# Kernel tuning notes

Hardware: AMD Instinct MI355X
Metric: run time of the kernel (lower is better)

The kernel has to match this reference:

```python
import jax, jax.numpy as jnp
import numpy as np

B, N, D, F, L, R = 16, 1024, 256, 128, 2, 2


def setup_inputs() -> dict:
    key = jax.random.key(0)
    ks = jax.random.split(key, 12)
    s = 0.05
    return {
        "node_embed": jax.random.normal(ks[0], (B, N, D), jnp.float32),
        "input_x": jax.random.normal(ks[1], (B, F), jnp.float32),
        "adj": jax.random.randint(ks[2], (R, B, N, N), 0, 2, jnp.int32),
        "WQi_w": jax.random.normal(ks[3], (L, F, F), jnp.float32) * s,
        "WQi_b": jnp.zeros((L, F), jnp.float32),
        "WQ_w": jax.random.normal(ks[4], (L, D + F, D), jnp.float32) * s,
        "WQ_b": jnp.zeros((L, D), jnp.float32),
        "WK_w": jax.random.normal(ks[5], (L, R, D + F, D), jnp.float32) * s,
        "WK_b": jnp.zeros((L, R, D), jnp.float32),
        "WV_w": jax.random.normal(ks[6], (L, R, D + F, D), jnp.float32) * s,
        "WV_b": jnp.zeros((L, R, D), jnp.float32),
        "WF_w": jax.random.normal(ks[7], (L, R * D, D), jnp.float32) * s,
        "WF_b": jnp.zeros((L, D), jnp.float32),
        "ln_g": jnp.ones((L, D), jnp.float32),
        "ln_b": jnp.zeros((L, D), jnp.float32),
    }


def _layer_norm(x, g, b, eps=1e-5):
    mu = jnp.mean(x, axis=-1, keepdims=True)
    var = jnp.var(x, axis=-1, keepdims=True)
    return (x - mu) * jax.lax.rsqrt(var + eps) * g + b


def reference(node_embed, input_x, adj, WQi_w, WQi_b, WQ_w, WQ_b,
              WK_w, WK_b, WV_w, WV_b, WF_w, WF_b, ln_g, ln_b):
    scale = 1.0 / (D ** 0.5)
    h = node_embed
    for l in range(L):
        # input feature projection, broadcast over nodes
        x1 = input_x @ WQi_w[l] + WQi_b[l]              # (B, F)
        x1 = jnp.broadcast_to(x1[:, None, :], (h.shape[0], h.shape[1], F))
        qc = jnp.concatenate([h, x1], axis=-1)          # (B, N, D+F)
        q = qc @ WQ_w[l] + WQ_b[l]                      # (B, N, D)
        outs = []
        for r in range(R):
            k = qc @ WK_w[l, r] + WK_b[l, r]            # (B, N, D)
            v = qc @ WV_w[l, r] + WV_b[l, r]            # (B, N, D)
            scores = jnp.einsum('bnd,bmd->bnm', q, k) * scale
            scores = jnp.where(adj[r] == 0, -1e9, scores)
            alpha = jax.nn.softmax(scores, axis=-1)
            outs.append(jnp.einsum('bnm,bmd->bnd', alpha, v))
        h_concat = jnp.concatenate(outs, axis=-1)       # (B, N, R*D)
        h_fused = jax.nn.relu(h_concat @ WF_w[l] + WF_b[l])
        h = _layer_norm(h + h_fused, ln_g[l], ln_b[l])
    return h
```

## Files before the change

kernel.cpp:

```cpp
#include <hip/hip_runtime.h>
#include <hip/hip_bf16.h>

#define BB 16
#define NN 1024
#define DD 256
#define FF_ 128
#define LL 2
#define RR 2
#define DF 384
#define MM (BB*NN)
#define NPROJ 1280
#define PK 768

typedef __attribute__((ext_vector_type(8))) short s16x8;
typedef __attribute__((ext_vector_type(4))) float f32x4;
typedef __attribute__((ext_vector_type(16))) float f32x16;
typedef __attribute__((ext_vector_type(2))) unsigned int u32x2;
typedef __attribute__((ext_vector_type(4))) unsigned int u32x4;
typedef __attribute__((ext_vector_type(4))) unsigned short us16x4;

__device__ __forceinline__ unsigned short f2bf(float f){
  unsigned u = __builtin_bit_cast(unsigned, f);
  u += 0x7fff + ((u >> 16) & 1);
  return (unsigned short)(u >> 16);
}

__device__ __forceinline__ void gload16(const void* g, void* l){
  __builtin_amdgcn_global_load_lds(
      (const __attribute__((address_space(1))) unsigned int*)g,
      (__attribute__((address_space(3))) unsigned int*)l, 16, 0, 0);
}

#define MFMA16(a,b,c) __builtin_amdgcn_mfma_f32_16x16x32_bf16((a),(b),(c),0,0,0)
#define MFMA32(a,b,c) __builtin_amdgcn_mfma_f32_32x32x16_bf16((a),(b),(c),0,0,0)

__global__ __launch_bounds__(256) void pack_adj(const int* __restrict__ adj,
                                                unsigned long long* __restrict__ bits){
  int w = threadIdx.x >> 6, lane = threadIdx.x & 63;
  size_t row = (size_t)blockIdx.x * 4 + w;
  const int* a = adj + row * NN;
  unsigned long long* brow = bits + row * 16;
  #pragma unroll
  for (int j = 0; j < 16; ++j){
    unsigned long long m = __ballot(a[j*64 + lane] != 0);
    if (lane == 0) brow[j] = m;
  }
}

#define PREP_WT   3840
#define PREP_WTF  1024
#define PREP_BALL 10
#define PREP_X1   16
#define PREP_H    2048
#define PREP_TOT  (PREP_WT+PREP_WTF+PREP_BALL+PREP_X1+PREP_H)

__global__ __launch_bounds__(256) void prep(
    const float* __restrict__ node, const float* __restrict__ inx,
    const float* __restrict__ WQi_w, const float* __restrict__ WQi_b,
    const float* __restrict__ WQ_w, const float* __restrict__ WK_w,
    const float* __restrict__ WV_w, const float* __restrict__ WQ_b,
    const float* __restrict__ WK_b, const float* __restrict__ WV_b,
    const float* __restrict__ WF_w,
    unsigned short* __restrict__ wtall, unsigned short* __restrict__ wtf,
    float* __restrict__ ball, unsigned short* __restrict__ x1bf,
    unsigned short* __restrict__ hbf){
  int bid = blockIdx.x, t = threadIdx.x;
  if (bid < PREP_WT){
    int o = bid*256 + t;
    int l = o / (NPROJ*DF); int oo = o - l*(NPROJ*DF);
    int n = oo / DF, k = oo - n*DF;
    const float* WQ = WQ_w + (size_t)l*DF*256;
    const float* WK = WK_w + (size_t)l*RR*DF*256;
    const float* WV = WV_w + (size_t)l*RR*DF*256;
    float v;
    if (n < 256)      v = WQ[(size_t)k*256 + n];
    else if (n < 768) v = WK[(size_t)((n-256)>>8)*(DF*256) + (size_t)k*256 + ((n-256)&255)];
    else              v = WV[(size_t)((n-768)>>8)*(DF*256) + (size_t)k*256 + ((n-768)&255)];
    wtall[o] = f2bf(v);
  } else if (bid < PREP_WT + PREP_WTF){
    int o = (bid - PREP_WT)*256 + t;
    int l = o >> 17; int oo = o & 131071;
    int n = oo >> 9, k = oo & 511;
    wtf[o] = f2bf(WF_w[(size_t)l*512*256 + (size_t)k*256 + n]);
  } else if (bid < PREP_WT + PREP_WTF + PREP_BALL){
    int o = (bid - PREP_WT - PREP_WTF)*256 + t;
    if (o < 2*NPROJ){
      int l = o / NPROJ, n = o - l*NPROJ;
      float v = (n < 256) ? WQ_b[l*256 + n]
              : (n < 768) ? WK_b[(size_t)l*512 + (n-256)]
                          : WV_b[(size_t)l*512 + (n-768)];
      ball[o] = v;
    }
  } else if (bid < PREP_WT + PREP_WTF + PREP_BALL + PREP_X1){
    int o = (bid - PREP_WT - PREP_WTF - PREP_BALL)*256 + t;
    int l = o >> 11, bj = o & 2047;
    int b = bj >> 7, j = bj & 127;
    const float* w = WQi_w + (size_t)l*FF_*FF_;
    float s = WQi_b[l*FF_ + j];
    for (int i = 0; i < FF_; ++i) s += inx[b*FF_ + i] * w[i*FF_ + j];
    x1bf[o] = f2bf(s);
  } else {
    int o = (bid - (PREP_TOT - PREP_H))*256 + t;
    const float4* src = (const float4*)node + (size_t)o*2;
    float4 a = src[0], c = src[1];
    uint4 pk;
    pk.x = (unsigned)f2bf(a.x) | ((unsigned)f2bf(a.y) << 16);
    pk.y = (unsigned)f2bf(a.z) | ((unsigned)f2bf(a.w) << 16);
    pk.z = (unsigned)f2bf(c.x) | ((unsigned)f2bf(c.y) << 16);
    pk.w = (unsigned)f2bf(c.z) | ((unsigned)f2bf(c.w) << 16);
    *(uint4*)(hbf + (size_t)o*8) = pk;
  }
}

__global__ __launch_bounds__(256) void gemm_big(const unsigned short* __restrict__ hbf,
    const unsigned short* __restrict__ x1l, const unsigned short* __restrict__ Wt,
    const float* __restrict__ bias, unsigned short* __restrict__ POUT,
    unsigned short* __restrict__ vtall){
  __shared__ unsigned short As[2][128*32];
  __shared__ unsigned short Bs[2][128*32];
  int t = threadIdx.x, lane = t & 63, w = t >> 6;
  int wr = w >> 1, wc = w & 1, l15 = lane & 15, lhi = lane >> 4;
  int bm = blockIdx.x, bn = blockIdx.y, bb = bm >> 3;
  f32x4 acc[4][4];
  #pragma unroll
  for (int m = 0; m < 4; ++m)
    #pragma unroll
    for (int n = 0; n < 4; ++n) acc[m][n] = (f32x4){0.f,0.f,0.f,0.f};

  auto STAGE = [&](int bi, int kk){
    #pragma unroll
    for (int i = 0; i < 2; ++i){
      int base = w*2048 + i*1024;
      int off = base + lane*16;
      int row = off >> 6, cb = off & 63;
      const char* asrc = (kk < 8)
        ? (const char*)hbf + ((size_t)(bm*128 + row)*256 + kk*32)*2 + cb
        : (const char*)x1l + ((size_t)bb*128 + (kk-8)*32)*2 + cb;
      gload16(asrc, (char*)As[bi] + base);
      gload16((const char*)Wt + ((size_t)(bn*128 + row)*DF + kk*32)*2 + cb,
              (char*)Bs[bi] + base);
    }
  };

  STAGE(0, 0);
  __syncthreads();
  for (int kk = 0; kk < 12; ++kk){
    int cur = kk & 1;
    if (kk + 1 < 12) STAGE(cur ^ 1, kk + 1);
    s16x8 af[4], bfr[4];
    #pragma unroll
    for (int m = 0; m < 4; ++m) af[m]  = *(const s16x8*)&As[cur][(wr*64 + m*16 + l15)*32 + lhi*8];
    #pragma unroll
    for (int n = 0; n < 4; ++n) bfr[n] = *(const s16x8*)&Bs[cur][(wc*64 + n*16 + l15)*32 + lhi*8];
    __builtin_amdgcn_s_setprio(1);
    #pragma unroll
    for (int m = 0; m < 4; ++m)
      #pragma unroll
      for (int n = 0; n < 4; ++n)
        acc[m][n] = MFMA16(af[m], bfr[n], acc[m][n]);
    __builtin_amdgcn_s_setprio(0);
    __syncthreads();
  }

  if (bn < 6){
    #pragma unroll
    for (int n = 0; n < 4; ++n){
      int gn = bn*128 + wc*64 + n*16 + l15;
      float bv = bias[gn];
      #pragma unroll
      for (int m = 0; m < 4; ++m){
        int gm = bm*128 + wr*64 + m*16 + lhi*4;
        #pragma unroll
        for (int i = 0; i < 4; ++i)
          POUT[(size_t)(gm + i)*PK + gn] = f2bf(acc[m][n][i] + bv);
      }
    }
  } else {
    #pragma unroll
    for (int n = 0; n < 4; ++n){
      int gn = bn*128 + wc*64 + n*16 + l15;
      float bv = bias[gn];
      int rv = gn - 768;
      int r = rv >> 8, d = rv & 255;
      #pragma unroll
      for (int m = 0; m < 4; ++m){
        int mb = (bm & 7)*128 + wr*64 + m*16 + lhi*4;
        us16x4 pk;
        #pragma unroll
        for (int i = 0; i < 4; ++i) pk[i] = f2bf(acc[m][n][i] + bv);
        *(us16x4*)(vtall + ((size_t)((r*16 + bb)*256 + d))*NN + mb) = pk;
      }
    }
  }
}

__global__ __launch_bounds__(512, 1) void attn9(const unsigned short* __restrict__ P,
    const unsigned short* __restrict__ VT, const unsigned long long* __restrict__ bits,
    unsigned short* __restrict__ hc){
  __shared__ char smem[131072];

  int t = threadIdx.x, lane = t & 63, w = t >> 6;
  int h = lane >> 5, l31 = lane & 31;
  int qsub = w >> 1, dh = w & 1;
  int F = blockIdx.x;
  int xcd = F & 7, j = F >> 3;
  int qt = j & 7;
  int gidx = xcd*4 + (j >> 3);
  int b = gidx & 15, r = gidx >> 4;
  const float C = 0.09016844f;

  size_t kcol = 256 + (size_t)r*256;
  const unsigned short* Vb = VT + ((size_t)(r*16 + b))*256*NN;
  int qrow = qt*128 + qsub*32 + l31;

  s16x8 qf[16];
  {
    const unsigned short* qp = P + ((size_t)(b*NN + qrow))*PK + h*8;
    #pragma unroll
    for (int d_ = 0; d_ < 16; ++d_) qf[d_] = *(const s16x8*)(qp + d_*16);
  }
  asm volatile("s_waitcnt vmcnt(0)" ::: "memory");

  f32x16 acc[4];
  #pragma unroll
  for (int dt = 0; dt < 4; ++dt)
    #pragma unroll
    for (int i = 0; i < 16; ++i) acc[dt][i] = 0.f;
  float mrow = -3e38f, lrow = 0.f;
  const unsigned long long* bitp = bits + ((size_t)(r*BB + b)*NN + qrow)*16;

  auto STAGE = [&](int buf, int kt){
    char* base = smem + buf*65536;
    #pragma unroll
    for (int i = 0; i < 4; ++i){
      int o = i*8192 + t*16;
      int kr = o >> 9, cb = o & 511;
      int lcb = cb ^ ((kr & 7) << 4);
      gload16((const char*)P + ((size_t)(b*NN + kt*64 + kr)*PK + kcol)*2 + lcb,
              base + o);
    }
    #pragma unroll
    for (int i = 0; i < 4; ++i){
      int o = i*8192 + t*16;
      int vr = o >> 7, cb = o & 127;
      int lcb = cb ^ ((vr & 7) << 4);
      gload16((const char*)Vb + ((size_t)vr*NN + kt*64)*2 + lcb,
              base + 32768 + o);
    }
  };

  STAGE(0, 0);

  for (int kt = 0; kt < 16; ++kt){
    int cur = kt & 1;
    unsigned long long mwv64 = bitp[kt];
    if (kt + 1 < 16){
      STAGE(cur ^ 1, kt + 1);
      asm volatile("s_waitcnt vmcnt(8)" ::: "memory");
    } else {
      asm volatile("s_waitcnt vmcnt(0)" ::: "memory");
    }
    __builtin_amdgcn_s_barrier();
    __builtin_amdgcn_sched_barrier(0);

    const char* Kc = smem + cur*65536;
    const char* Vc = smem + cur*65536 + 32768;

    #pragma unroll
    for (int s = 0; s < 2; ++s){
      f32x16 st;
      #pragma unroll
      for (int i = 0; i < 16; ++i) st[i] = 0.f;
      int krow = s*32 + l31;
      int swzk = (krow & 7) << 4;
      const char* kbase = Kc + krow*512;
      #pragma unroll
      for (int d_ = 0; d_ < 16; ++d_){
        s16x8 kf = *(const s16x8*)(kbase + ((d_*32 + h*16) ^ swzk));
        st = MFMA32(kf, qf[d_], st);
      }

      unsigned mw = (unsigned)(mwv64 >> (s*32));
      float tm = -3e38f;
      #pragma unroll
      for (int rr = 0; rr < 16; ++rr){
        int kb = (rr & 3) + 8*(rr >> 2) + 4*h;
        float sv = st[rr] * C;
        sv = ((mw >> kb) & 1u) ? sv : -1.443e9f;
        st[rr] = sv;
        tm = fmaxf(tm, sv);
      }
      tm = fmaxf(tm, __shfl_xor(tm, 32));
      if (tm > mrow + 10.f){
        float f = exp2f(mrow - tm);
        mrow = tm;
        lrow *= f;
        #pragma unroll
        for (int dt = 0; dt < 4; ++dt)
          #pragma unroll
          for (int i = 0; i < 16; ++i) acc[dt][i] *= f;
      }
      float rs = 0.f;
      #pragma unroll
      for (int rr = 0; rr < 16; ++rr){
        float e = exp2f(st[rr] - mrow);
        st[rr] = e;
        rs += e;
      }
      rs += __shfl_xor(rs, 32);
      lrow += rs;

      unsigned pk[8];
      #pragma unroll
      for (int p = 0; p < 8; ++p){
        unsigned rpk;
        float lo = st[p*2], hi = st[p*2+1];
        asm("v_cvt_pk_bf16_f32 %0, %1, %2" : "=v"(rpk) : "v"(lo), "v"(hi));
        pk[p] = rpk;
      }
      unsigned sA = h ? pk[0] : pk[2], sB = h ? pk[1] : pk[3];
      unsigned sC = h ? pk[4] : pk[6], sD = h ? pk[5] : pk[7];
      unsigned rxA = (unsigned)__shfl_xor((int)sA, 32);
      unsigned rxB = (unsigned)__shfl_xor((int)sB, 32);
      unsigned rxC = (unsigned)__shfl_xor((int)sC, 32);
      unsigned rxD = (unsigned)__shfl_xor((int)sD, 32);
      u32x4 pv0, pv1;
      pv0[0] = h ? rxA : pk[0]; pv0[1] = h ? rxB : pk[1];
      pv0[2] = h ? pk[2] : rxA; pv0[3] = h ? pk[3] : rxB;
      pv1[0] = h ? rxC : pk[4]; pv1[1] = h ? rxD : pk[5];
      pv1[2] = h ? pk[6] : rxC; pv1[3] = h ? pk[7] : rxD;
      s16x8 pa0 = __builtin_bit_cast(s16x8, pv0);
      s16x8 pa1 = __builtin_bit_cast(s16x8, pv1);

      #pragma unroll
      for (int dt = 0; dt < 4; ++dt){
        int vr = dh*128 + dt*32 + l31;
        int swzv = (vr & 7) << 4;
        const char* vbase = Vc + vr*128;
        s16x8 vf0 = *(const s16x8*)(vbase + (((2*s)*32 + h*16) ^ swzv));
        acc[dt] = MFMA32(vf0, pa0, acc[dt]);
        s16x8 vf1 = *(const s16x8*)(vbase + (((2*s+1)*32 + h*16) ^ swzv));
        acc[dt] = MFMA32(vf1, pa1, acc[dt]);
      }
    }

    __builtin_amdgcn_s_barrier();
  }

  float inv = 1.f / lrow;
  unsigned short* hrow = hc + ((size_t)(b*NN + qrow))*(RR*DD) + r*DD;
  #pragma unroll
  for (int dt = 0; dt < 4; ++dt){
    #pragma unroll
    for (int g = 0; g < 4; ++g){
      float a0 = acc[dt][g*4+0]*inv, a1 = acc[dt][g*4+1]*inv;
      float a2 = acc[dt][g*4+2]*inv, a3 = acc[dt][g*4+3]*inv;
      unsigned r0, r1;
      asm("v_cvt_pk_bf16_f32 %0, %1, %2" : "=v"(r0) : "v"(a0), "v"(a1));
      asm("v_cvt_pk_bf16_f32 %0, %1, %2" : "=v"(r1) : "v"(a2), "v"(a3));
      int d = dh*128 + dt*32 + 8*g + 4*h;
      u32x2 pv; pv[0] = r0; pv[1] = r1;
      *(u32x2*)(hrow + d) = pv;
    }
  }
}

__global__ __launch_bounds__(256) void gemm_ff(const unsigned short* __restrict__ A,
    const unsigned short* __restrict__ Wt, const float* __restrict__ bias,
    float* __restrict__ out){
  __shared__ unsigned short As[2][128*32];
  __shared__ unsigned short Bs[2][128*32];
  int t = threadIdx.x, lane = t & 63, w = t >> 6;
  int wr = w >> 1, wc = w & 1, l15 = lane & 15, lhi = lane >> 4;
  int bm = blockIdx.x, bn = blockIdx.y;
  f32x4 acc[4][4];
  #pragma unroll
  for (int m = 0; m < 4; ++m)
    #pragma unroll
    for (int n = 0; n < 4; ++n) acc[m][n] = (f32x4){0.f,0.f,0.f,0.f};

  auto STAGE = [&](int bi, int kk){
    #pragma unroll
    for (int i = 0; i < 2; ++i){
      int base = w*2048 + i*1024;
      int off = base + lane*16;
      int row = off >> 6, cb = off & 63;
      gload16((const char*)A  + ((size_t)(bm*128 + row)*512 + kk*32)*2 + cb,
              (char*)As[bi] + base);
      gload16((const char*)Wt + ((size_t)(bn*128 + row)*512 + kk*32)*2 + cb,
              (char*)Bs[bi] + base);
    }
  };

  STAGE(0, 0);
  __syncthreads();
  for (int kk = 0; kk < 16; ++kk){
    int cur = kk & 1;
    if (kk + 1 < 16) STAGE(cur ^ 1, kk + 1);
    s16x8 af[4], bfr[4];
    #pragma unroll
    for (int m = 0; m < 4; ++m) af[m]  = *(const s16x8*)&As[cur][(wr*64 + m*16 + l15)*32 + lhi*8];
    #pragma unroll
    for (int n = 0; n < 4; ++n) bfr[n] = *(const s16x8*)&Bs[cur][(wc*64 + n*16 + l15)*32 + lhi*8];
    __builtin_amdgcn_s_setprio(1);
    #pragma unroll
    for (int m = 0; m < 4; ++m)
      #pragma unroll
      for (int n = 0; n < 4; ++n)
        acc[m][n] = MFMA16(af[m], bfr[n], acc[m][n]);
    __builtin_amdgcn_s_setprio(0);
    __syncthreads();
  }

  #pragma unroll
  for (int n = 0; n < 4; ++n){
    int gn = bn*128 + wc*64 + n*16 + l15;
    float bv = bias[gn];
    #pragma unroll
    for (int m = 0; m < 4; ++m){
      int gm = bm*128 + wr*64 + m*16 + lhi*4;
      #pragma unroll
      for (int i = 0; i < 4; ++i)
        out[(size_t)(gm + i)*DD + gn] = acc[m][n][i] + bv;
    }
  }
}

template<int WRITEH>
__global__ __launch_bounds__(256) void ln_res2(const float* __restrict__ ff,
    const float* __restrict__ hin, const float* __restrict__ g,
    const float* __restrict__ bv, float* __restrict__ hout,
    unsigned short* __restrict__ hbf){
  int w = threadIdx.x >> 6, lane = threadIdx.x & 63;
  size_t row = (size_t)blockIdx.x * 4 + w;
  f32x4 fv = *(const f32x4*)(ff  + row*DD + lane*4);
  f32x4 hv = *(const f32x4*)(hin + row*DD + lane*4);
  float x[4], s = 0.f, ss = 0.f;
  #pragma unroll
  for (int j = 0; j < 4; ++j){ x[j] = fmaxf(fv[j], 0.f) + hv[j]; s += x[j]; ss += x[j]*x[j]; }
  #pragma unroll
  for (int xm = 1; xm < 64; xm <<= 1){ s += __shfl_xor(s, xm); ss += __shfl_xor(ss, xm); }
  float mu = s * (1.f/256.f);
  float var = ss * (1.f/256.f) - mu*mu;
  float rstd = rsqrtf(var + 1e-5f);
  f32x4 o;
  #pragma unroll
  for (int j = 0; j < 4; ++j){ int c = lane*4 + j; o[j] = (x[j]-mu)*rstd*g[c] + bv[c]; }
  *(f32x4*)(hout + row*DD + lane*4) = o;
  if (WRITEH){
    uint2 pv;
    pv.x = (unsigned)f2bf(o[0]) | ((unsigned)f2bf(o[1]) << 16);
    pv.y = (unsigned)f2bf(o[2]) | ((unsigned)f2bf(o[3]) << 16);
    *(uint2*)(hbf + row*DD + lane*4) = pv;
  }
}

extern "C" void kernel_launch(void* const* d_in, const int* in_sizes, int n_in,
                              void* d_out, int out_size, void* d_ws, size_t ws_size,
                              hipStream_t stream){
  (void)in_sizes; (void)n_in; (void)out_size; (void)ws_size;
  const float* node  = (const float*)d_in[0];
  const float* inx   = (const float*)d_in[1];
  const int*   adj   = (const int*)d_in[2];
  const float* WQi_w = (const float*)d_in[3];
  const float* WQi_b = (const float*)d_in[4];
  const float* WQ_w  = (const float*)d_in[5];
  const float* WQ_b  = (const float*)d_in[6];
  const float* WK_w  = (const float*)d_in[7];
  const float* WK_b  = (const float*)d_in[8];
  const float* WV_w  = (const float*)d_in[9];
  const float* WV_b  = (const float*)d_in[10];
  const float* WF_w  = (const float*)d_in[11];
  const float* WF_b  = (const float*)d_in[12];
  const float* ln_g  = (const float*)d_in[13];
  const float* ln_b  = (const float*)d_in[14];
  float* hout = (float*)d_out;

  char* wsp = (char*)d_ws;
  auto alloc = [&](size_t n){ char* p = wsp; wsp += (n + 255) & ~(size_t)255; return p; };
  unsigned long long* bits = (unsigned long long*)alloc((size_t)RR*BB*NN*16*8);
  unsigned short* wtall = (unsigned short*)alloc((size_t)2*NPROJ*DF*2);
  unsigned short* wtf   = (unsigned short*)alloc((size_t)2*DD*512*2);
  float*          ball  = (float*)alloc((size_t)2*NPROJ*4);
  unsigned short* x1bf  = (unsigned short*)alloc((size_t)2*BB*FF_*2);
  unsigned short* hbf   = (unsigned short*)alloc((size_t)MM*DD*2);
  unsigned short* POUT  = (unsigned short*)alloc((size_t)MM*PK*2);
  unsigned short* vtall = (unsigned short*)alloc((size_t)RR*BB*DD*NN*2);
  unsigned short* hc    = (unsigned short*)alloc((size_t)MM*512*2);
  float*          ffo   = (float*)alloc((size_t)MM*DD*4);

  pack_adj<<<RR*BB*NN/4, 256, 0, stream>>>(adj, bits);
  prep<<<PREP_TOT, 256, 0, stream>>>(node, inx, WQi_w, WQi_b, WQ_w, WK_w, WV_w,
                                     WQ_b, WK_b, WV_b, WF_w,
                                     wtall, wtf, ball, x1bf, hbf);

  for (int l = 0; l < LL; ++l){
    gemm_big<<<dim3(128,10), 256, 0, stream>>>(hbf, x1bf + (size_t)l*BB*FF_,
        wtall + (size_t)l*NPROJ*DF, ball + (size_t)l*NPROJ, POUT, vtall);

    attn9<<<256, 512, 0, stream>>>(POUT, vtall, bits, hc);

    gemm_ff<<<dim3(128,2), 256, 0, stream>>>(hc, wtf + (size_t)l*DD*512, WF_b + l*DD, ffo);

    if (l == 0) ln_res2<1><<<MM/4, 256, 0, stream>>>(ffo, node, ln_g, ln_b, hout, hbf);
    else        ln_res2<0><<<MM/4, 256, 0, stream>>>(ffo, (const float*)hout,
                                                     ln_g + DD, ln_b + DD, hout, nullptr);
  }
}
```

Before: 302.3 us.

## Fold softmax scale into WQ, stage mask bits in LDS, interleave score MFMAs

The softmax scale is folded into the WQ weights and bias during prep, which removes a per-element multiply in the attention loop. Each block preloads its adjacency bitmask tile into an extra 16KB of LDS, replacing a per-iteration global load. The two key sub-tiles' QK MFMA chains are now issued interleaved so they can overlap, and the max and sum reductions use trees instead of serial chains. The cost is more LDS and more live registers, and the scaled Q is rounded to bf16 after scaling.

New measurement: 303.8 us. No clear change (+0.5%).

```diff
diff --git a/kernel.cpp b/kernel.cpp
--- a/kernel.cpp
+++ b/kernel.cpp
@@ -11,6 +11,7 @@
 #define MM (BB*NN)
 #define NPROJ 1280
 #define PK 768
+#define CSC 0.09016844f
 
 typedef __attribute__((ext_vector_type(8))) short s16x8;
 typedef __attribute__((ext_vector_type(4))) float f32x4;
@@ -73,7 +74,7 @@
     const float* WK = WK_w + (size_t)l*RR*DF*256;
     const float* WV = WV_w + (size_t)l*RR*DF*256;
     float v;
-    if (n < 256)      v = WQ[(size_t)k*256 + n];
+    if (n < 256)      v = WQ[(size_t)k*256 + n] * CSC;
     else if (n < 768) v = WK[(size_t)((n-256)>>8)*(DF*256) + (size_t)k*256 + ((n-256)&255)];
     else              v = WV[(size_t)((n-768)>>8)*(DF*256) + (size_t)k*256 + ((n-768)&255)];
     wtall[o] = f2bf(v);
@@ -86,7 +87,7 @@
     int o = (bid - PREP_WT - PREP_WTF)*256 + t;
     if (o < 2*NPROJ){
       int l = o / NPROJ, n = o - l*NPROJ;
-      float v = (n < 256) ? WQ_b[l*256 + n]
+      float v = (n < 256) ? WQ_b[l*256 + n] * CSC
               : (n < 768) ? WK_b[(size_t)l*512 + (n-256)]
                           : WV_b[(size_t)l*512 + (n-768)];
       ball[o] = v;
@@ -194,10 +195,10 @@
   }
 }
 
-__global__ __launch_bounds__(512, 1) void attn9(const unsigned short* __restrict__ P,
+__global__ __launch_bounds__(512, 1) void attn10(const unsigned short* __restrict__ P,
     const unsigned short* __restrict__ VT, const unsigned long long* __restrict__ bits,
     unsigned short* __restrict__ hc){
-  __shared__ char smem[131072];
+  __shared__ char smem[147456];
 
   int t = threadIdx.x, lane = t & 63, w = t >> 6;
   int h = lane >> 5, l31 = lane & 31;
@@ -207,7 +208,6 @@
   int qt = j & 7;
   int gidx = xcd*4 + (j >> 3);
   int b = gidx & 15, r = gidx >> 4;
-  const float C = 0.09016844f;
 
   size_t kcol = 256 + (size_t)r*256;
   const unsigned short* Vb = VT + ((size_t)(r*16 + b))*256*NN;
@@ -219,7 +219,17 @@
     #pragma unroll
     for (int d_ = 0; d_ < 16; ++d_) qf[d_] = *(const s16x8*)(qp + d_*16);
   }
-  asm volatile("s_waitcnt vmcnt(0)" ::: "memory");
+
+  {
+    const unsigned long long* bb0 = bits + ((size_t)(r*BB + b)*NN + qt*128)*16;
+    unsigned long long* ml = (unsigned long long*)(smem + 131072);
+    #pragma unroll
+    for (int i = 0; i < 4; ++i){
+      int idx = t + i*512;
+      int kt = idx >> 7, row = idx & 127;
+      ml[kt*128 + row] = bb0[(size_t)row*16 + kt];
+    }
+  }
 
   f32x16 acc[4];
   #pragma unroll
@@ -227,7 +237,6 @@
     #pragma unroll
     for (int i = 0; i < 16; ++i) acc[dt][i] = 0.f;
   float mrow = -3e38f, lrow = 0.f;
-  const unsigned long long* bitp = bits + ((size_t)(r*BB + b)*NN + qrow)*16;
 
   auto STAGE = [&](int buf, int kt){
     char* base = smem + buf*65536;
@@ -250,10 +259,10 @@
   };
 
   STAGE(0, 0);
+  __syncthreads();
 
   for (int kt = 0; kt < 16; ++kt){
     int cur = kt & 1;
-    unsigned long long mwv64 = bitp[kt];
     if (kt + 1 < 16){
       STAGE(cur ^ 1, kt + 1);
       asm volatile("s_waitcnt vmcnt(8)" ::: "memory");
@@ -263,33 +272,39 @@
     __builtin_amdgcn_s_barrier();
     __builtin_amdgcn_sched_barrier(0);
 
+    unsigned long long mwv64 = *(const unsigned long long*)
+        (smem + 131072 + kt*1024 + (qsub*32 + l31)*8);
+
     const char* Kc = smem + cur*65536;
     const char* Vc = smem + cur*65536 + 32768;
 
-    #pragma unroll
-    for (int s = 0; s < 2; ++s){
-      f32x16 st;
-      #pragma unroll
-      for (int i = 0; i < 16; ++i) st[i] = 0.f;
-      int krow = s*32 + l31;
-      int swzk = (krow & 7) << 4;
-      const char* kbase = Kc + krow*512;
-      #pragma unroll
-      for (int d_ = 0; d_ < 16; ++d_){
-        s16x8 kf = *(const s16x8*)(kbase + ((d_*32 + h*16) ^ swzk));
-        st = MFMA32(kf, qf[d_], st);
-      }
-
-      unsigned mw = (unsigned)(mwv64 >> (s*32));
-      float tm = -3e38f;
+    f32x16 st0, st1;
+    #pragma unroll
+    for (int i = 0; i < 16; ++i){ st0[i] = 0.f; st1[i] = 0.f; }
+    int swzk = (l31 & 7) << 4;
+    const char* kb0 = Kc + l31*512;
+    const char* kb1 = Kc + (32 + l31)*512;
+    #pragma unroll
+    for (int d_ = 0; d_ < 16; ++d_){
+      int co = (d_*32 + h*16) ^ swzk;
+      s16x8 kf0 = *(const s16x8*)(kb0 + co);
+      s16x8 kf1 = *(const s16x8*)(kb1 + co);
+      st0 = MFMA32(kf0, qf[d_], st0);
+      st1 = MFMA32(kf1, qf[d_], st1);
+    }
+
+    auto PROC = [&](f32x16 st, unsigned mw, int vcol){
       #pragma unroll
       for (int rr = 0; rr < 16; ++rr){
         int kb = (rr & 3) + 8*(rr >> 2) + 4*h;
-        float sv = st[rr] * C;
-        sv = ((mw >> kb) & 1u) ? sv : -1.443e9f;
-        st[rr] = sv;
-        tm = fmaxf(tm, sv);
+        st[rr] = ((mw >> kb) & 1u) ? st[rr] : -1.443e9f;
       }
+      float t8[8];
+      #pragma unroll
+      for (int p = 0; p < 8; ++p) t8[p] = fmaxf(st[p], st[p+8]);
+      #pragma unroll
+      for (int p = 0; p < 4; ++p) t8[p] = fmaxf(t8[p], t8[p+4]);
+      float tm = fmaxf(fmaxf(t8[0], t8[1]), fmaxf(t8[2], t8[3]));
       tm = fmaxf(tm, __shfl_xor(tm, 32));
       if (tm > mrow + 10.f){
         float f = exp2f(mrow - tm);
@@ -300,13 +315,13 @@
           #pragma unroll
           for (int i = 0; i < 16; ++i) acc[dt][i] *= f;
       }
-      float rs = 0.f;
-      #pragma unroll
-      for (int rr = 0; rr < 16; ++rr){
-        float e = exp2f(st[rr] - mrow);
-        st[rr] = e;
-        rs += e;
-      }
+      #pragma unroll
+      for (int rr = 0; rr < 16; ++rr) st[rr] = exp2f(st[rr] - mrow);
+      #pragma unroll
+      for (int p = 0; p < 8; ++p) t8[p] = st[p] + st[p+8];
+      #pragma unroll
+      for (int p = 0; p < 4; ++p) t8[p] = t8[p] + t8[p+4];
+      float rs = (t8[0] + t8[1]) + (t8[2] + t8[3]);
       rs += __shfl_xor(rs, 32);
       lrow += rs;
 
@@ -337,12 +352,14 @@
         int vr = dh*128 + dt*32 + l31;
         int swzv = (vr & 7) << 4;
         const char* vbase = Vc + vr*128;
-        s16x8 vf0 = *(const s16x8*)(vbase + (((2*s)*32 + h*16) ^ swzv));
+        s16x8 vf0 = *(const s16x8*)(vbase + ((vcol + h*16) ^ swzv));
         acc[dt] = MFMA32(vf0, pa0, acc[dt]);
-        s16x8 vf1 = *(const s16x8*)(vbase + (((2*s+1)*32 + h*16) ^ swzv));
+        s16x8 vf1 = *(const s16x8*)(vbase + ((vcol + 32 + h*16) ^ swzv));
         acc[dt] = MFMA32(vf1, pa1, acc[dt]);
       }
-    }
+    };
+    PROC(st0, (unsigned)mwv64, 0);
+    PROC(st1, (unsigned)(mwv64 >> 32), 64);
 
     __builtin_amdgcn_s_barrier();
   }
@@ -498,7 +515,7 @@
     gemm_big<<<dim3(128,10), 256, 0, stream>>>(hbf, x1bf + (size_t)l*BB*FF_,
         wtall + (size_t)l*NPROJ*DF, ball + (size_t)l*NPROJ, POUT, vtall);
 
-    attn9<<<256, 512, 0, stream>>>(POUT, vtall, bits, hc);
+    attn10<<<256, 512, 0, stream>>>(POUT, vtall, bits, hc);
 
     gemm_ff<<<dim3(128,2), 256, 0, stream>>>(hc, wtf + (size_t)l*DD*512, WF_b + l*DD, ffo);
 
```
